# Performance work log

Hardware: AMD Instinct MI355X
Metric: run time of the kernel (lower is better)

Reference implementation:

```python
import jax, jax.numpy as jnp
import numpy as np

DIM = 768
HEADS = 12
HEAD_DIM = DIM // HEADS
SCALE = HEAD_DIM ** -0.5


def setup_inputs() -> dict:
    key = jax.random.key(0)
    k1, k2, k3, k4, k5 = jax.random.split(key, 5)
    B, N = 4, 2048
    x = jax.random.normal(k1, (B, N, DIM), dtype=jnp.float32)
    # qkv Linear: weight [3*dim, dim], bias [3*dim]
    w_qkv = jax.random.normal(k2, (3 * DIM, DIM), dtype=jnp.float32) * (DIM ** -0.5)
    b_qkv = jax.random.normal(k3, (3 * DIM,), dtype=jnp.float32) * 0.01
    # proj Linear: weight [dim, dim], bias [dim]
    w_proj = jax.random.normal(k4, (DIM, DIM), dtype=jnp.float32) * (DIM ** -0.5)
    b_proj = jax.random.normal(k5, (DIM,), dtype=jnp.float32) * 0.01
    return {"x": x, "w_qkv": w_qkv, "b_qkv": b_qkv, "w_proj": w_proj, "b_proj": b_proj}


def reference(x, w_qkv, b_qkv, w_proj, b_proj):
    B, N, C = x.shape
    qkv = (jnp.einsum('bnc,oc->bno', x, w_qkv) + b_qkv)
    qkv = qkv.reshape(B, N, 3, HEADS, HEAD_DIM).transpose(2, 0, 3, 1, 4)
    q, k, v = qkv[0], qkv[1], qkv[2]
    attn = jnp.einsum('bhqd,bhkd->bhqk', q, k) * SCALE
    attn = jax.nn.softmax(attn, axis=-1)
    out = jnp.einsum('bhqk,bhkd->bhqd', attn, v)  # [B, H, N, Dh]
    out = out.transpose(0, 2, 1, 3).reshape(B, N, C)
    # dropout is identity in eval mode
    return jnp.einsum('bnc,oc->bno', out, w_proj) + b_proj
```

## Files before the change

### kernel.cpp

```cpp
#include <hip/hip_runtime.h>
#include <hip/hip_bf16.h>

using bf16 = __hip_bfloat16;
typedef __bf16 bf16x8 __attribute__((ext_vector_type(8)));
typedef short short4v __attribute__((ext_vector_type(4)));
typedef short short8v __attribute__((ext_vector_type(8)));
typedef float float4v __attribute__((ext_vector_type(4)));

#define DIM   768
#define NH    12
#define HD    64
#define SEQ   2048
#define BATCH 4
#define TOK   (BATCH * SEQ)
#define SCALE_QL2E 0.18033688011112042f

#define NX  (TOK * DIM)
#define NWQ (3 * DIM * DIM)
#define NWP (DIM * DIM)

__device__ __forceinline__ short f2bf(float f) {
  union { bf16 h; short s; } u;
  u.h = __float2bfloat16(f);
  return u.s;
}

union frag8 { short4v h[2]; short8v s; bf16x8 b; unsigned u[4]; };

__device__ __forceinline__ void async_copy16(const bf16* g, short* l) {
  __builtin_amdgcn_global_load_lds(
      (const __attribute__((address_space(1))) unsigned int*)g,
      (__attribute__((address_space(3))) unsigned int*)l, 16, 0, 0);
}
__device__ __forceinline__ void async_copy4(const bf16* g, short* l) {
  __builtin_amdgcn_global_load_lds(
      (const __attribute__((address_space(1))) unsigned int*)g,
      (__attribute__((address_space(3))) unsigned int*)l, 4, 0, 0);
}

#define BARRIER __builtin_amdgcn_s_barrier()
#define LGKM0 asm volatile("s_waitcnt lgkmcnt(0)" ::: "memory")
#define VW0 asm volatile("s_waitcnt vmcnt(0)" ::: "memory")
#define NOSTG (void)0
#define NOVW  (void)0

__global__ void __launch_bounds__(256)
cvt3(const float* __restrict__ a, bf16* __restrict__ oa, long na,
     const float* __restrict__ b, bf16* __restrict__ ob, long nb,
     const float* __restrict__ c, bf16* __restrict__ oc, long nc) {
  const long i = ((long)blockIdx.x * 256 + threadIdx.x) * 8;
  const float* src; bf16* dst; long off;
  if (i < na)                { src = a; dst = oa; off = i; }
  else if (i < na + nb)      { src = b; dst = ob; off = i - na; }
  else if (i < na + nb + nc) { src = c; dst = oc; off = i - na - nb; }
  else return;
  const float4v x0 = *(const float4v*)(src + off);
  const float4v x1 = *(const float4v*)(src + off + 4);
  short8v r;
  r[0] = f2bf(x0[0]); r[1] = f2bf(x0[1]); r[2] = f2bf(x0[2]); r[3] = f2bf(x0[3]);
  r[4] = f2bf(x1[0]); r[5] = f2bf(x1[1]); r[6] = f2bf(x1[2]); r[7] = f2bf(x1[3]);
  *(short8v*)(dst + off) = r;
}

#define STGP(s, p)                                                            \
  async_copy16(pa + (p) * 32,             &As[s][t * 8]);                     \
  async_copy16(pa + 64 * DIM + (p) * 32,  &As[s][2048 + t * 8]);              \
  async_copy16(pb + (p) * 32,             &Bs[s][t * 8]);                     \
  async_copy16(pb + 64 * DIM + (p) * 32,  &Bs[s][2048 + t * 8]);              \
  async_copy16(pb + 128 * DIM + (p) * 32, &Bs[s][4096 + t * 8]);              \
  async_copy16(pb + 192 * DIM + (p) * 32, &Bs[s][6144 + t * 8]);              \
  async_copy4 (pb3 + (p) * 32,            &Bs[s][8192 + t * 2]);              \
  async_copy4 (pb3 + 16 * DIM + (p) * 32, &Bs[s][8704 + t * 2])

#define PHASE(CUR, STG_, VW_) {                                               \
  bf16x8 af[4], bfv[9];                                                       \
  _Pragma("unroll") for (int mf_ = 0; mf_ < 4; ++mf_)                         \
    af[mf_] = *(const bf16x8*)&As[CUR][mf_ * 512 + arow];                     \
  _Pragma("unroll") for (int nf_ = 0; nf_ < 9; ++nf_)                         \
    bfv[nf_] = *(const bf16x8*)&Bs[CUR][nf_ * 512 + brow];                    \
  STG_; BARRIER; LGKM0;                                                       \
  __builtin_amdgcn_s_setprio(1);                                              \
  _Pragma("unroll") for (int mf_ = 0; mf_ < 4; ++mf_)                         \
  _Pragma("unroll") for (int nf_ = 0; nf_ < 9; ++nf_)                         \
    acc[mf_][nf_] = __builtin_amdgcn_mfma_f32_16x16x32_bf16(                  \
        af[mf_], bfv[nf_], acc[mf_][nf_], 0, 0, 0);                           \
  __builtin_amdgcn_s_setprio(0); VW_; BARRIER; }

__global__ void __launch_bounds__(256, 2)
gemm_qkv(const bf16* __restrict__ X, const bf16* __restrict__ W,
         const float* __restrict__ bias,
         bf16* __restrict__ qb, bf16* __restrict__ kb, bf16* __restrict__ vb) {
  __shared__ short As[2][128 * 32];
  __shared__ short Bs[2][288 * 32];
  const int t = threadIdx.x;
  const int w = t >> 6, l = t & 63, lr = l & 15, q = l >> 4;
  const int wm = w >> 1, wn = w & 1;

  const int orig = blockIdx.x;
  const int swz = (orig & 7) * 64 + (orig >> 3);
  const int tm = swz >> 3, tn = swz & 7;
  const int row0 = tm * 128, col0 = tn * 288;

  const int sr = t >> 2;
  const int scol = (((t & 3) << 3) ^ (((sr >> 1) & 3) << 3));
  const bf16* pa  = X + (size_t)(row0 + sr) * DIM + scol;
  const bf16* pb  = W + (size_t)(col0 + sr) * DIM + scol;
  const int r3 = t >> 4;
  const int c3 = ((t & 15) << 1) ^ (((r3 >> 1) & 3) << 3);
  const bf16* pb3 = W + (size_t)(col0 + 256 + r3) * DIM + c3;

  const int acol = ((q << 3) ^ (((lr >> 1) & 3) << 3));
  const int arow = (wm * 64 + lr) * 32 + acol;
  const int brow = (wn * 144 + lr) * 32 + acol;

  float4v acc[4][9] = {};

  STGP(0, 0);
  VW0; BARRIER;

#pragma unroll 1
  for (int k = 0; k < 22; k += 2) {
    PHASE(0, STGP(1, k + 1), VW0)
    PHASE(1, STGP(0, k + 2), VW0)
  }
  PHASE(0, STGP(1, 23), VW0)
  PHASE(1, NOSTG,       NOVW)

#pragma unroll
  for (int nf = 0; nf < 9; ++nf) {
    const int gn = col0 + wn * 144 + nf * 16 + lr;
    const int which = gn / DIM;
    const int cc = gn - which * DIM;
    const int hh = cc >> 6, dd = cc & 63;
    const float bv = bias[gn];
#pragma unroll
    for (int mf = 0; mf < 4; ++mf) {
      const int gm0 = row0 + wm * 64 + mf * 16 + (q << 2);
      const int b = gm0 >> 11, n0 = gm0 & 2047;
      if (which == 2) {
        short4v pv;
#pragma unroll
        for (int r = 0; r < 4; ++r) pv[r] = f2bf(acc[mf][nf][r] + bv);
        *(short4v*)&vb[((size_t)(b * NH + hh) * HD + dd) * SEQ + n0] = pv;
      } else {
        bf16* dst = (which == 0) ? qb : kb;
        const float sc = (which == 0) ? SCALE_QL2E : 1.0f;
#pragma unroll
        for (int r = 0; r < 4; ++r)
          dst[((size_t)(b * NH + hh) * SEQ + n0 + r) * HD + dd] =
              __float2bfloat16((acc[mf][nf][r] + bv) * sc);
      }
    }
  }
}

#define STG_KV(bb, k1)                                                        \
  async_copy16(Kb + (size_t)((k1) + drow) * HD + skey,       &KV[bb][t * 8]); \
  async_copy16(Kb + (size_t)((k1) + 32 + drow) * HD + skey,  &KV[bb][2048 + t * 8]); \
  async_copy16(Vb + (size_t)drow * SEQ + (k1) + skey,        &KV[bb][4096 + t * 8]); \
  async_copy16(Vb + (size_t)(32 + drow) * SEQ + (k1) + skey, &KV[bb][6144 + t * 8])

#define S_STEP(BK_) {                                                         \
  const short* Bf_ = KV[BK_];                                                 \
  __builtin_amdgcn_s_setprio(1);                                              \
  _Pragma("unroll") for (int jn = 0; jn < 4; ++jn) {                          \
    bf16x8 kf[2];                                                             \
    _Pragma("unroll") for (int kq = 0; kq < 2; ++kq)                          \
      kf[kq] = *(const bf16x8*)&Bf_[(jn * 16 + lr) * 64 +                     \
                                    (((kq * 32) + (q << 3)) ^ key8)];         \
    _Pragma("unroll") for (int it = 0; it < 2; ++it)                          \
    _Pragma("unroll") for (int kq = 0; kq < 2; ++kq)                          \
      s[jn][it] = __builtin_amdgcn_mfma_f32_16x16x32_bf16(kf[kq],             \
                      qf[it][kq], s[jn][it], 0, 0, 0);                        \
  }                                                                           \
  __builtin_amdgcn_s_setprio(0); }

#define PV_STEP(PF_, BP_) {                                                   \
  const short* Bv_ = KV[BP_] + 4096;                                          \
  __builtin_amdgcn_s_setprio(1);                                              \
  _Pragma("unroll") for (int c4 = 0; c4 < 2; ++c4) {                          \
    _Pragma("unroll") for (int dj = 0; dj < 4; ++dj) {                        \
      frag8 vf;                                                               \
      vf.h[0] = *(const short4v*)&Bv_[(dj * 16 + lr) * 64 +                   \
                                      ((c4 * 32 + (q << 2)) ^ key8)];         \
      vf.h[1] = *(const short4v*)&Bv_[(dj * 16 + lr) * 64 +                   \
                                      ((c4 * 32 + 16 + (q << 2)) ^ key8)];    \
      _Pragma("unroll") for (int it = 0; it < 2; ++it)                        \
        o[it][dj] = __builtin_amdgcn_mfma_f32_16x16x32_bf16(PF_[c4][it].b,    \
                        vf.b, o[it][dj], 0, 0, 0);                            \
    }                                                                         \
    _Pragma("unroll") for (int it = 0; it < 2; ++it)                          \
      lacc[it] = __builtin_amdgcn_mfma_f32_16x16x32_bf16(PF_[c4][it].b,       \
                     ones.b, lacc[it], 0, 0, 0);                              \
  }                                                                           \
  __builtin_amdgcn_s_setprio(0); }

#define SM_STEP(PF_)                                                          \
  _Pragma("unroll") for (int it = 0; it < 2; ++it)                            \
  _Pragma("unroll") for (int c4 = 0; c4 < 2; ++c4)                            \
  _Pragma("unroll") for (int r = 0; r < 4; ++r) {                             \
    PF_[c4][it].s[r]     = f2bf(__builtin_amdgcn_exp2f(s[2 * c4][it][r]));    \
    PF_[c4][it].s[4 + r] = f2bf(__builtin_amdgcn_exp2f(s[2 * c4 + 1][it][r]));\
  }

#define FA_BODY(BK_, BP_, BN_, PFP_, PFC_, TILE1_) {                          \
  float4v s[4][2] = {};                                                       \
  S_STEP(BK_);                                                                \
  PV_STEP(PFP_, BP_);                                                         \
  STG_KV(BN_, (TILE1_) * 64);                                                 \
  SM_STEP(PFC_);                                                              \
  VW0; BARRIER; }

__global__ void __launch_bounds__(256, 3)
flash_attn(const bf16* __restrict__ Qp, const bf16* __restrict__ Kp,
           const bf16* __restrict__ Vtp, bf16* __restrict__ Op) {
  const int bh = blockIdx.y, qt = blockIdx.x;
  const int t = threadIdx.x, w = t >> 6, l = t & 63, lr = l & 15, q = l >> 4;
  __shared__ short KV[3][8192];

  const bf16* Qb = Qp  + (size_t)(bh * SEQ + qt * 128) * HD;
  const bf16* Kb = Kp  + (size_t)bh * SEQ * HD;
  const bf16* Vb = Vtp + (size_t)bh * HD * SEQ;

  const int drow = t >> 3;
  const int skey = (((t & 7) ^ drow) & 7) * 8;

  bf16x8 qf[2][2];
#pragma unroll
  for (int it = 0; it < 2; ++it)
#pragma unroll
    for (int kq = 0; kq < 2; ++kq)
      qf[it][kq] = *(const bf16x8*)(Qb + (size_t)(w * 32 + it * 16 + lr) * HD +
                                    kq * 32 + q * 8);

  const int key8 = (lr & 7) << 3;

  frag8 ones;
#pragma unroll
  for (int r = 0; r < 8; ++r) ones.s[r] = (short)0x3F80;

  float4v o[2][4] = {};
  float4v lacc[2] = {};
  frag8 pfA[2][2], pfB[2][2];

  STG_KV(0, 0);
  VW0; BARRIER;

  {
    float4v s[4][2] = {};
    S_STEP(0);
    STG_KV(1, 64);
    SM_STEP(pfA);
    VW0; BARRIER;
  }

  int bK = 1;
#pragma unroll 1
  for (int kt = 1; kt < 31; kt += 2) {
    const int bP = (bK == 0) ? 2 : bK - 1;
    const int bN = (bK == 2) ? 0 : bK + 1;
    FA_BODY(bK, bP, bN, pfA, pfB, kt + 1)
    FA_BODY(bN, bK, bP, pfB, pfA, kt + 2)
    bK = bP;
  }

  {
    float4v s[4][2] = {};
    S_STEP(1);
    PV_STEP(pfA, 0);
    SM_STEP(pfB);
    PV_STEP(pfB, 1);
  }

  const int b = bh / NH, h = bh - b * NH;
#pragma unroll
  for (int it = 0; it < 2; ++it)
#pragma unroll
    for (int r = 0; r < 4; ++r) {
      const float linv = 1.0f / lacc[it][r];
      const int grow = b * SEQ + qt * 128 + w * 32 + it * 16 + (q << 2) + r;
      bf16* orow = Op + (size_t)grow * DIM + h * HD;
#pragma unroll
      for (int dj = 0; dj < 4; ++dj)
        orow[dj * 16 + lr] = __float2bfloat16(o[it][dj][r] * linv);
    }
}

#define PRJ_STG(s, p)                                                         \
  async_copy16(pa + (p) * 32,             &Asp[s][t * 8]);                    \
  async_copy16(pb + (p) * 32,             &Bsp[s][t * 8]);                    \
  async_copy16(pb + 64 * DIM + (p) * 32,  &Bsp[s][2048 + t * 8]);             \
  async_copy16(pb + 128 * DIM + (p) * 32, &Bsp[s][4096 + t * 8])

#define PRJ_PHASE(CUR, STG_, VW_) {                                           \
  bf16x8 af[2], bfv[6];                                                       \
  _Pragma("unroll") for (int mf_ = 0; mf_ < 2; ++mf_)                         \
    af[mf_] = *(const bf16x8*)&Asp[CUR][mf_ * 512 + arow];                    \
  _Pragma("unroll") for (int nf_ = 0; nf_ < 6; ++nf_)                         \
    bfv[nf_] = *(const bf16x8*)&Bsp[CUR][nf_ * 512 + brow];                   \
  STG_; BARRIER; LGKM0;                                                       \
  __builtin_amdgcn_s_setprio(1);                                              \
  _Pragma("unroll") for (int mf_ = 0; mf_ < 2; ++mf_)                         \
  _Pragma("unroll") for (int nf_ = 0; nf_ < 6; ++nf_)                         \
    acc[mf_][nf_] = __builtin_amdgcn_mfma_f32_16x16x32_bf16(                  \
        af[mf_], bfv[nf_], acc[mf_][nf_], 0, 0, 0);                           \
  __builtin_amdgcn_s_setprio(0); VW_; BARRIER; }

__global__ void __launch_bounds__(256, 2)
gemm_proj(const bf16* __restrict__ A, const bf16* __restrict__ W,
          const float* __restrict__ bias, float* __restrict__ out) {
  __shared__ short Asp[2][64 * 32];
  __shared__ short Bsp[2][192 * 32];
  const int t = threadIdx.x;
  const int w = t >> 6, l = t & 63, lr = l & 15, q = l >> 4;
  const int wm = w >> 1, wn = w & 1;

  const int orig = blockIdx.x;
  const int swz = (orig & 7) * 64 + (orig >> 3);
  const int tm = swz >> 2, tn = swz & 3;
  const int row0 = tm * 64, col0 = tn * 192;

  const int sr = t >> 2;
  const int scol = (((t & 3) << 3) ^ (((sr >> 1) & 3) << 3));
  const bf16* pa = A + (size_t)(row0 + sr) * DIM + scol;
  const bf16* pb = W + (size_t)(col0 + sr) * DIM + scol;

  const int acol = ((q << 3) ^ (((lr >> 1) & 3) << 3));
  const int arow = (wm * 32 + lr) * 32 + acol;
  const int brow = (wn * 96 + lr) * 32 + acol;

  float4v acc[2][6] = {};

  PRJ_STG(0, 0);
  VW0; BARRIER;

#pragma unroll 1
  for (int k = 0; k < 22; k += 2) {
    PRJ_PHASE(0, PRJ_STG(1, k + 1), VW0)
    PRJ_PHASE(1, PRJ_STG(0, k + 2), VW0)
  }
  PRJ_PHASE(0, PRJ_STG(1, 23), VW0)
  PRJ_PHASE(1, NOSTG,          NOVW)

#pragma unroll
  for (int nf = 0; nf < 6; ++nf) {
    const int gn = col0 + wn * 96 + nf * 16 + lr;
    const float bv = bias[gn];
#pragma unroll
    for (int mf = 0; mf < 2; ++mf) {
#pragma unroll
      for (int r = 0; r < 4; ++r) {
        const int gm = row0 + wm * 32 + mf * 16 + (q << 2) + r;
        out[(size_t)gm * DIM + gn] = acc[mf][nf][r] + bv;
      }
    }
  }
}

extern "C" void kernel_launch(void* const* d_in, const int* in_sizes, int n_in,
                              void* d_out, int out_size, void* d_ws, size_t ws_size,
                              hipStream_t stream) {
  const float* x      = (const float*)d_in[0];
  const float* w_qkv  = (const float*)d_in[1];
  const float* b_qkv  = (const float*)d_in[2];
  const float* w_proj = (const float*)d_in[3];
  const float* b_proj = (const float*)d_in[4];
  float* out = (float*)d_out;

  const size_t perbuf = (size_t)BATCH * NH * SEQ * HD;
  bf16* qb  = (bf16*)d_ws;
  bf16* kb  = qb + perbuf;
  bf16* vb  = kb + perbuf;
  bf16* ao  = vb + perbuf;
  bf16* xb  = ao + perbuf;
  bf16* wqb = xb + (size_t)NX;
  bf16* wpb = wqb + (size_t)NWQ;

  const int cvt_blocks = (NX + NWQ + NWP) / 8 / 256;
  cvt3<<<cvt_blocks, 256, 0, stream>>>(x, xb, NX, w_qkv, wqb, NWQ, w_proj, wpb, NWP);
  gemm_qkv <<<dim3(512), 256, 0, stream>>>(xb, wqb, b_qkv, qb, kb, vb);
  flash_attn<<<dim3(SEQ / 128, BATCH * NH), 256, 0, stream>>>(qb, kb, vb, ao);
  gemm_proj <<<dim3(512), 256, 0, stream>>>(ao, wpb, b_proj, out);
}
```

Measured before the change: 196.2 us.

## Split flash-attention work across 8 waves with 16 query rows each

```diff
diff --git a/kernel.cpp b/kernel.cpp
--- a/kernel.cpp
+++ b/kernel.cpp
@@ -155,10 +155,8 @@
 }
 
 #define STG_KV(bb, k1)                                                        \
-  async_copy16(Kb + (size_t)((k1) + drow) * HD + skey,       &KV[bb][t * 8]); \
-  async_copy16(Kb + (size_t)((k1) + 32 + drow) * HD + skey,  &KV[bb][2048 + t * 8]); \
-  async_copy16(Vb + (size_t)drow * SEQ + (k1) + skey,        &KV[bb][4096 + t * 8]); \
-  async_copy16(Vb + (size_t)(32 + drow) * SEQ + (k1) + skey, &KV[bb][6144 + t * 8])
+  async_copy16(Kb + (size_t)((k1) + drow) * HD + skey,  &KV[bb][t * 8]);      \
+  async_copy16(Vb + (size_t)drow * SEQ + (k1) + skey,   &KV[bb][4096 + t * 8])
 
 #define S_STEP(BK_) {                                                         \
   const short* Bf_ = KV[BK_];                                                 \
@@ -168,10 +166,9 @@
     _Pragma("unroll") for (int kq = 0; kq < 2; ++kq)                          \
       kf[kq] = *(const bf16x8*)&Bf_[(jn * 16 + lr) * 64 +                     \
                                     (((kq * 32) + (q << 3)) ^ key8)];         \
-    _Pragma("unroll") for (int it = 0; it < 2; ++it)                          \
     _Pragma("unroll") for (int kq = 0; kq < 2; ++kq)                          \
-      s[jn][it] = __builtin_amdgcn_mfma_f32_16x16x32_bf16(kf[kq],             \
-                      qf[it][kq], s[jn][it], 0, 0, 0);                        \
+      s[jn] = __builtin_amdgcn_mfma_f32_16x16x32_bf16(kf[kq], qf[kq],         \
+                                                      s[jn], 0, 0, 0);        \
   }                                                                           \
   __builtin_amdgcn_s_setprio(0); }
 
@@ -185,33 +182,30 @@
                                       ((c4 * 32 + (q << 2)) ^ key8)];         \
       vf.h[1] = *(const short4v*)&Bv_[(dj * 16 + lr) * 64 +                   \
                                       ((c4 * 32 + 16 + (q << 2)) ^ key8)];    \
-      _Pragma("unroll") for (int it = 0; it < 2; ++it)                        \
-        o[it][dj] = __builtin_amdgcn_mfma_f32_16x16x32_bf16(PF_[c4][it].b,    \
-                        vf.b, o[it][dj], 0, 0, 0);                            \
+      o[dj] = __builtin_amdgcn_mfma_f32_16x16x32_bf16(PF_[c4].b, vf.b,        \
+                                                      o[dj], 0, 0, 0);        \
     }                                                                         \
-    _Pragma("unroll") for (int it = 0; it < 2; ++it)                          \
-      lacc[it] = __builtin_amdgcn_mfma_f32_16x16x32_bf16(PF_[c4][it].b,       \
-                     ones.b, lacc[it], 0, 0, 0);                              \
+    lacc = __builtin_amdgcn_mfma_f32_16x16x32_bf16(PF_[c4].b, ones.b,         \
+                                                   lacc, 0, 0, 0);            \
   }                                                                           \
   __builtin_amdgcn_s_setprio(0); }
 
 #define SM_STEP(PF_)                                                          \
-  _Pragma("unroll") for (int it = 0; it < 2; ++it)                            \
   _Pragma("unroll") for (int c4 = 0; c4 < 2; ++c4)                            \
   _Pragma("unroll") for (int r = 0; r < 4; ++r) {                             \
-    PF_[c4][it].s[r]     = f2bf(__builtin_amdgcn_exp2f(s[2 * c4][it][r]));    \
-    PF_[c4][it].s[4 + r] = f2bf(__builtin_amdgcn_exp2f(s[2 * c4 + 1][it][r]));\
+    PF_[c4].s[r]     = f2bf(__builtin_amdgcn_exp2f(s[2 * c4][r]));            \
+    PF_[c4].s[4 + r] = f2bf(__builtin_amdgcn_exp2f(s[2 * c4 + 1][r]));        \
   }
 
 #define FA_BODY(BK_, BP_, BN_, PFP_, PFC_, TILE1_) {                          \
-  float4v s[4][2] = {};                                                       \
+  float4v s[4] = {};                                                          \
   S_STEP(BK_);                                                                \
   PV_STEP(PFP_, BP_);                                                         \
   STG_KV(BN_, (TILE1_) * 64);                                                 \
   SM_STEP(PFC_);                                                              \
   VW0; BARRIER; }
 
-__global__ void __launch_bounds__(256, 3)
+__global__ void __launch_bounds__(512, 6)
 flash_attn(const bf16* __restrict__ Qp, const bf16* __restrict__ Kp,
            const bf16* __restrict__ Vtp, bf16* __restrict__ Op) {
   const int bh = blockIdx.y, qt = blockIdx.x;
@@ -225,13 +219,10 @@
   const int drow = t >> 3;
   const int skey = (((t & 7) ^ drow) & 7) * 8;
 
-  bf16x8 qf[2][2];
-#pragma unroll
-  for (int it = 0; it < 2; ++it)
-#pragma unroll
-    for (int kq = 0; kq < 2; ++kq)
-      qf[it][kq] = *(const bf16x8*)(Qb + (size_t)(w * 32 + it * 16 + lr) * HD +
-                                    kq * 32 + q * 8);
+  bf16x8 qf[2];
+#pragma unroll
+  for (int kq = 0; kq < 2; ++kq)
+    qf[kq] = *(const bf16x8*)(Qb + (size_t)(w * 16 + lr) * HD + kq * 32 + q * 8);
 
   const int key8 = (lr & 7) << 3;
 
@@ -239,15 +230,15 @@
 #pragma unroll
   for (int r = 0; r < 8; ++r) ones.s[r] = (short)0x3F80;
 
-  float4v o[2][4] = {};
-  float4v lacc[2] = {};
-  frag8 pfA[2][2], pfB[2][2];
+  float4v o[4] = {};
+  float4v lacc = {};
+  frag8 pfA[2], pfB[2];
 
   STG_KV(0, 0);
   VW0; BARRIER;
 
   {
-    float4v s[4][2] = {};
+    float4v s[4] = {};
     S_STEP(0);
     STG_KV(1, 64);
     SM_STEP(pfA);
@@ -265,7 +256,7 @@
   }
 
   {
-    float4v s[4][2] = {};
+    float4v s[4] = {};
     S_STEP(1);
     PV_STEP(pfA, 0);
     SM_STEP(pfB);
@@ -274,16 +265,14 @@
 
   const int b = bh / NH, h = bh - b * NH;
 #pragma unroll
-  for (int it = 0; it < 2; ++it)
-#pragma unroll
-    for (int r = 0; r < 4; ++r) {
-      const float linv = 1.0f / lacc[it][r];
-      const int grow = b * SEQ + qt * 128 + w * 32 + it * 16 + (q << 2) + r;
-      bf16* orow = Op + (size_t)grow * DIM + h * HD;
-#pragma unroll
-      for (int dj = 0; dj < 4; ++dj)
-        orow[dj * 16 + lr] = __float2bfloat16(o[it][dj][r] * linv);
-    }
+  for (int r = 0; r < 4; ++r) {
+    const float linv = 1.0f / lacc[r];
+    const int grow = b * SEQ + qt * 128 + w * 16 + (q << 2) + r;
+    bf16* orow = Op + (size_t)grow * DIM + h * HD;
+#pragma unroll
+    for (int dj = 0; dj < 4; ++dj)
+      orow[dj * 16 + lr] = __float2bfloat16(o[dj][r] * linv);
+  }
 }
 
 #define PRJ_STG(s, p)                                                         \
@@ -379,6 +368,6 @@
   const int cvt_blocks = (NX + NWQ + NWP) / 8 / 256;
   cvt3<<<cvt_blocks, 256, 0, stream>>>(x, xb, NX, w_qkv, wqb, NWQ, w_proj, wpb, NWP);
   gemm_qkv <<<dim3(512), 256, 0, stream>>>(xb, wqb, b_qkv, qb, kb, vb);
-  flash_attn<<<dim3(SEQ / 128, BATCH * NH), 256, 0, stream>>>(qb, kb, vb, ao);
+  flash_attn<<<dim3(SEQ / 128, BATCH * NH), 512, 0, stream>>>(qb, kb, vb, ao);
   gemm_proj <<<dim3(512), 256, 0, stream>>>(ao, wpb, b_proj, out);
 }
```

New measurement: 249.3 us. 1.27x slower.
